# Kernel tuning notes

Hardware: AMD Instinct MI355X
Metric: run time of the kernel (lower is better)

The kernel has to match this reference:

```python
import jax, jax.numpy as jnp
import numpy as np
import math

B, S, E, H, F = 2, 2048, 1024, 16, 4096
D = E // H
EPS = 1e-5


def _layernorm(x, g, b):
    mu = jnp.mean(x, axis=-1, keepdims=True)
    var = jnp.mean(jnp.square(x - mu), axis=-1, keepdims=True)
    return (x - mu) * jax.lax.rsqrt(var + EPS) * g + b


def _xavier(k, fan_in, fan_out):
    limit = math.sqrt(6.0 / (fan_in + fan_out))
    return jax.random.uniform(k, (fan_in, fan_out), jnp.float32, -limit, limit)


def setup_inputs() -> dict:
    key = jax.random.key(0)
    ks = jax.random.split(key, 8)
    x = jax.random.normal(ks[0], (B, S, E), jnp.float32)
    # causal mask: 1 where attendable, 0 where masked (masked_fill at mask==0)
    mask = jnp.tril(jnp.ones((S, S), jnp.int32))[None, None]  # [1,1,S,S]
    return {
        "x": x,
        "mask": mask,
        "Wq": _xavier(ks[1], E, E), "bq": jnp.zeros((E,), jnp.float32),
        "Wk": _xavier(ks[2], E, E), "bk": jnp.zeros((E,), jnp.float32),
        "Wv": _xavier(ks[3], E, E), "bv": jnp.zeros((E,), jnp.float32),
        "Wo": _xavier(ks[4], E, E), "bo": jnp.zeros((E,), jnp.float32),
        "W1": _xavier(ks[5], E, F), "b1": jnp.zeros((F,), jnp.float32),
        "W2": _xavier(ks[6], F, E), "b2": jnp.zeros((E,), jnp.float32),
        "ln1_g": jnp.ones((E,), jnp.float32), "ln1_b": jnp.zeros((E,), jnp.float32),
        "ln2_g": jnp.ones((E,), jnp.float32), "ln2_b": jnp.zeros((E,), jnp.float32),
    }


def reference(x, mask, Wq, bq, Wk, bk, Wv, bv, Wo, bo, W1, b1, W2, b2,
              ln1_g, ln1_b, ln2_g, ln2_b):
    n = _layernorm(x, ln1_g, ln1_b)
    # project and split heads: [B,S,E] -> [B,H,S,D]
    def heads(w, b):
        return (n @ w + b).reshape(B, S, H, D).transpose(0, 2, 1, 3)
    Q, K, V = heads(Wq, bq), heads(Wk, bk), heads(Wv, bv)
    scores = jnp.einsum('bhsd,bhtd->bhst', Q, K) / math.sqrt(D)  # [B,H,S,S]
    scores = jnp.where(mask == 0, jnp.float32(-1e9), scores)
    attn = jax.nn.softmax(scores, axis=-1)
    ctx = jnp.einsum('bhst,bhtd->bhsd', attn, V)
    ctx = ctx.transpose(0, 2, 1, 3).reshape(B, S, E)
    attn_out = ctx @ Wo + bo
    x = _layernorm(x + attn_out, ln2_g, ln2_b)
    ffn = jax.nn.gelu(x @ W1 + b1, approximate=False) @ W2 + b2
    return x + ffn
```

## Files before the change

### kernel.cpp

```cpp
#include <hip/hip_runtime.h>
#include <cmath>

typedef unsigned short u16;
typedef unsigned int u32;
typedef __bf16 bf16x8 __attribute__((ext_vector_type(8)));
typedef float f32x4 __attribute__((ext_vector_type(4)));

#define SEQ 2048
#define EMB 1024
#define NHEAD 16
#define HDIM 64
#define FFDIM 4096
#define NBATCH 2
#define QKVLD 3072
#define PWS 68

#define QSCALE 0.18033688011112042f

__device__ __forceinline__ u16 f2bf(float f) {
  u32 u = __float_as_uint(f);
  u32 r = u + 0x7fffu + ((u >> 16) & 1u);
  return (u16)(r >> 16);
}

__device__ __forceinline__ float ex2(float x) {
#if __has_builtin(__builtin_amdgcn_exp2f)
  return __builtin_amdgcn_exp2f(x);
#else
  return exp2f(x);
#endif
}

__device__ __forceinline__ float geluf(float x) {
  float u = 0.7978845608028654f * (x + 0.044715f * x * x * x);
  float e = ex2(2.8853900817779268f * u);
  return x - x / (e + 1.0f);
}

__device__ __forceinline__ void gload16(const void* g, void* l) {
  __builtin_amdgcn_global_load_lds(
      (const __attribute__((address_space(1))) unsigned int*)g,
      (__attribute__((address_space(3))) unsigned int*)l, 16, 0, 0);
}

__device__ __forceinline__ u32 lds_addr(const void* p) {
  return (u32)(size_t)(const __attribute__((address_space(3))) void*)p;
}

template <int IMM>
__device__ __forceinline__ bf16x8 dsr16(u32 a) {
  bf16x8 r;
  asm volatile("ds_read_b128 %0, %1 offset:%2" : "=v"(r) : "v"(a), "n"(IMM));
  return r;
}

__global__ __launch_bounds__(256)
void wtrans_kernel(const float* __restrict__ W, u16* __restrict__ WT, int K, int N) {
  __shared__ float tile[32][33];
  int tx = threadIdx.x & 31, ty = threadIdx.x >> 5;
  int n0 = blockIdx.x * 32, k0 = blockIdx.y * 32;
#pragma unroll
  for (int i = 0; i < 32; i += 8)
    tile[ty + i][tx] = W[(size_t)(k0 + ty + i) * N + (n0 + tx)];
  __syncthreads();
#pragma unroll
  for (int i = 0; i < 32; i += 8)
    WT[(size_t)(n0 + ty + i) * K + (k0 + tx)] = f2bf(tile[tx][ty + i]);
}

__global__ __launch_bounds__(256)
void wtrans4_kernel(const float* __restrict__ W0, const float* __restrict__ W1_,
                    const float* __restrict__ W2_, const float* __restrict__ W3,
                    u16* __restrict__ Dqkv, u16* __restrict__ Do) {
  __shared__ float tile[32][33];
  int z = blockIdx.z;
  const float* W = (z == 0) ? W0 : (z == 1) ? W1_ : (z == 2) ? W2_ : W3;
  u16* D = (z < 3) ? (Dqkv + (size_t)z * EMB * EMB) : Do;
  int tx = threadIdx.x & 31, ty = threadIdx.x >> 5;
  int n0 = blockIdx.x * 32, k0 = blockIdx.y * 32;
#pragma unroll
  for (int i = 0; i < 32; i += 8)
    tile[ty + i][tx] = W[(size_t)(k0 + ty + i) * EMB + (n0 + tx)];
  __syncthreads();
#pragma unroll
  for (int i = 0; i < 32; i += 8)
    D[(size_t)(n0 + ty + i) * EMB + (k0 + tx)] = f2bf(tile[tx][ty + i]);
}

__global__ __launch_bounds__(256)
void vtrans_kernel(const u16* __restrict__ QKV, u16* __restrict__ Vt) {
  __shared__ u16 tile[64 * 72];
  int bh = blockIdx.y, b = bh >> 4, h = bh & 15;
  int s0 = blockIdx.x * 64;
  const u16* src = QKV + (size_t)b * SEQ * QKVLD + 2048 + (size_t)h * HDIM;
  int tid = threadIdx.x;
#pragma unroll
  for (int cc = 0; cc < 2; ++cc) {
    int c = tid + cc * 256;
    int s = c >> 3, d0 = (c & 7) * 8;
    uint4 v = *(const uint4*)(src + (size_t)(s0 + s) * QKVLD + d0);
    *(uint4*)(&tile[s * 72 + d0]) = v;
  }
  __syncthreads();
  u16* dst = Vt + (size_t)bh * HDIM * SEQ;
#pragma unroll
  for (int cc = 0; cc < 2; ++cc) {
    int c = tid + cc * 256;
    int d = c >> 3, t0l = (c & 7) * 8;
    union { uint4 u; u16 s[8]; } ou;
#pragma unroll
    for (int j = 0; j < 8; ++j) ou.s[j] = tile[(t0l + j) * 72 + d];
    *(uint4*)(dst + (size_t)d * SEQ + s0 + t0l) = ou.u;
  }
}

__global__ __launch_bounds__(256)
void ln_kernel(const float* __restrict__ in, const float* __restrict__ gamma,
               const float* __restrict__ beta, u16* __restrict__ outb) {
  int w = threadIdx.x >> 6, lane = threadIdx.x & 63;
  int row = blockIdx.x * 4 + w;
  size_t base = (size_t)row * EMB;
  float4 v[4];
  float s = 0.f, q = 0.f;
#pragma unroll
  for (int j = 0; j < 4; ++j) {
    v[j] = *(const float4*)(in + base + j * 256 + lane * 4);
    s += v[j].x + v[j].y + v[j].z + v[j].w;
    q += v[j].x * v[j].x + v[j].y * v[j].y + v[j].z * v[j].z + v[j].w * v[j].w;
  }
#pragma unroll
  for (int off = 1; off < 64; off <<= 1) {
    s += __shfl_xor(s, off);
    q += __shfl_xor(q, off);
  }
  float mean = s * (1.0f / EMB);
  float var = q * (1.0f / EMB) - mean * mean;
  float rstd = rsqrtf(var + 1e-5f);
#pragma unroll
  for (int j = 0; j < 4; ++j) {
    int c = j * 256 + lane * 4;
    float4 g4 = *(const float4*)(gamma + c);
    float4 b4 = *(const float4*)(beta + c);
    ushort4 ob;
    ob.x = f2bf((v[j].x - mean) * rstd * g4.x + b4.x);
    ob.y = f2bf((v[j].y - mean) * rstd * g4.y + b4.y);
    ob.z = f2bf((v[j].z - mean) * rstd * g4.z + b4.z);
    ob.w = f2bf((v[j].w - mean) * rstd * g4.w + b4.w);
    *(ushort4*)(outb + base + c) = ob;
  }
}

__global__ __launch_bounds__(256)
void ln2f_kernel(const float* __restrict__ p, size_t pstride,
                 const float* __restrict__ bias, const float* __restrict__ resid,
                 const float* __restrict__ gamma, const float* __restrict__ beta,
                 u16* __restrict__ outb, float* __restrict__ outf) {
  int w = threadIdx.x >> 6, lane = threadIdx.x & 63;
  int row = blockIdx.x * 4 + w;
  size_t base = (size_t)row * EMB;
  float4 v[4];
  float s = 0.f, q = 0.f;
#pragma unroll
  for (int j = 0; j < 4; ++j) {
    int c = j * 256 + lane * 4;
    float4 a = *(const float4*)(p + base + c);
    float4 b = *(const float4*)(p + pstride + base + c);
    float4 r = *(const float4*)(resid + base + c);
    float4 bb = *(const float4*)(bias + c);
    v[j].x = a.x + b.x + r.x + bb.x;
    v[j].y = a.y + b.y + r.y + bb.y;
    v[j].z = a.z + b.z + r.z + bb.z;
    v[j].w = a.w + b.w + r.w + bb.w;
    s += v[j].x + v[j].y + v[j].z + v[j].w;
    q += v[j].x * v[j].x + v[j].y * v[j].y + v[j].z * v[j].z + v[j].w * v[j].w;
  }
#pragma unroll
  for (int off = 1; off < 64; off <<= 1) {
    s += __shfl_xor(s, off);
    q += __shfl_xor(q, off);
  }
  float mean = s * (1.0f / EMB);
  float var = q * (1.0f / EMB) - mean * mean;
  float rstd = rsqrtf(var + 1e-5f);
#pragma unroll
  for (int j = 0; j < 4; ++j) {
    int c = j * 256 + lane * 4;
    float4 g4 = *(const float4*)(gamma + c);
    float4 b4 = *(const float4*)(beta + c);
    float y0 = (v[j].x - mean) * rstd * g4.x + b4.x;
    float y1 = (v[j].y - mean) * rstd * g4.y + b4.y;
    float y2 = (v[j].z - mean) * rstd * g4.z + b4.z;
    float y3 = (v[j].w - mean) * rstd * g4.w + b4.w;
    ushort4 ob;
    ob.x = f2bf(y0); ob.y = f2bf(y1); ob.z = f2bf(y2); ob.w = f2bf(y3);
    *(ushort4*)(outb + base + c) = ob;
    *(float4*)(outf + base + c) = make_float4(y0, y1, y2, y3);
  }
}

__global__ __launch_bounds__(256)
void reduce2_kernel(const float* __restrict__ p, size_t pstride,
                    const float* __restrict__ bias, const float* __restrict__ resid,
                    float* __restrict__ out, int ncols) {
  size_t i = ((size_t)blockIdx.x * 256 + threadIdx.x) * 4;
  float4 a = *(const float4*)(p + i);
  float4 b = *(const float4*)(p + pstride + i);
  float4 r = *(const float4*)(resid + i);
  int col = (int)(i & (size_t)(ncols - 1));
  float4 bb = *(const float4*)(bias + col);
  float4 o;
  o.x = a.x + b.x + r.x + bb.x;
  o.y = a.y + b.y + r.y + bb.y;
  o.z = a.z + b.z + r.z + bb.z;
  o.w = a.w + b.w + r.w + bb.w;
  *(float4*)(out + i) = o;
}

__global__ __launch_bounds__(256)
void gemm_bt(const u16* __restrict__ A, const u16* __restrict__ BT,
             const float* __restrict__ bias, const float* __restrict__ bias2,
             const float* __restrict__ bias3, void* __restrict__ out,
             const float* __restrict__ resid, int M, int N, int K,
             int mode, float scale, int ksplit,
             float* __restrict__ partial, size_t pstride) {
  __shared__ __align__(16) u16 As[128 * 64];
  __shared__ __align__(16) u16 Bs[128 * 64];
  int tid = threadIdx.x;
  int lane = tid & 63, w = tid >> 6;
  int wm = w >> 1, wn = w & 1;
  int g = lane >> 4, lr = lane & 15;
  int m0 = blockIdx.y * 128, n0 = blockIdx.x * 128;
  int z = blockIdx.z;
  int kbeg = z * ksplit, kend = kbeg + ksplit;

  f32x4 acc[4][4];
#pragma unroll
  for (int mt = 0; mt < 4; ++mt)
#pragma unroll
    for (int nt = 0; nt < 4; ++nt) {
      acc[mt][nt][0] = 0.f; acc[mt][nt][1] = 0.f;
      acc[mt][nt][2] = 0.f; acc[mt][nt][3] = 0.f;
    }

  size_t ao[4], bo_[4];
  int lo[4];
#pragma unroll
  for (int cc = 0; cc < 4; ++cc) {
    int c = tid + cc * 256;
    int row = c >> 3, slot = c & 7;
    int gc = slot ^ (row & 7);
    ao[cc] = (size_t)(m0 + row) * K + gc * 8;
    bo_[cc] = (size_t)(n0 + row) * K + gc * 8;
    lo[cc] = c * 8;
  }
  int swz[2];
#pragma unroll
  for (int kk = 0; kk < 2; ++kk) swz[kk] = ((kk * 4 + g) ^ (lr & 7)) * 8;

  for (int k0 = kbeg; k0 < kend; k0 += 64) {
    __syncthreads();
#pragma unroll
    for (int cc = 0; cc < 4; ++cc) gload16(A + ao[cc] + k0, As + lo[cc]);
#pragma unroll
    for (int cc = 0; cc < 4; ++cc) gload16(BT + bo_[cc] + k0, Bs + lo[cc]);
    __syncthreads();
#pragma unroll
    for (int kk = 0; kk < 2; ++kk) {
      bf16x8 af[4], bfr[4];
#pragma unroll
      for (int mt = 0; mt < 4; ++mt)
        af[mt] = *(const bf16x8*)(As + (wm * 64 + mt * 16 + lr) * 64 + swz[kk]);
#pragma unroll
      for (int nt = 0; nt < 4; ++nt)
        bfr[nt] = *(const bf16x8*)(Bs + (wn * 64 + nt * 16 + lr) * 64 + swz[kk]);
#pragma unroll
      for (int mt = 0; mt < 4; ++mt)
#pragma unroll
        for (int nt = 0; nt < 4; ++nt)
          acc[mt][nt] = __builtin_amdgcn_mfma_f32_16x16x32_bf16(af[mt], bfr[nt], acc[mt][nt], 0, 0, 0);
    }
  }

  float* pz = partial + (size_t)z * pstride;
#pragma unroll
  for (int mt = 0; mt < 4; ++mt) {
    int row = m0 + wm * 64 + mt * 16 + g * 4;
#pragma unroll
    for (int nt = 0; nt < 4; ++nt) {
      int col = n0 + wn * 64 + nt * 16 + lr;
      float bcol;
      if (mode == 3) {
        int which = col >> 10;
        const float* bp = (which == 0) ? bias : (which == 1) ? bias2 : bias3;
        bcol = bp[col & 1023];
      } else if (mode != 4) {
        bcol = bias[col];
      } else {
        bcol = 0.f;
      }
#pragma unroll
      for (int r = 0; r < 4; ++r) {
        float vacc = acc[mt][nt][r] + bcol;
        size_t idx = (size_t)(row + r) * N + col;
        if (mode == 0)      ((u16*)out)[idx] = f2bf(vacc * scale);
        else if (mode == 1) ((u16*)out)[idx] = f2bf(geluf(vacc));
        else if (mode == 2) ((float*)out)[idx] = vacc + resid[idx];
        else if (mode == 3) ((u16*)out)[idx] = f2bf(col < 1024 ? vacc * QSCALE : vacc);
        else                pz[idx] = vacc;
      }
    }
  }
}


#define BARM __builtin_amdgcn_s_barrier()
#define VMWS asm volatile("s_waitcnt vmcnt(%0)" ::"n"(4 + RA))
#define VMW0 asm volatile("s_waitcnt vmcnt(0)")
#define NOSTG ((void)0)
#define NOWT ((void)0)

#define STG_A(t, d, kh)                                                       \
  { _Pragma("unroll")                                                         \
    for (int j = 0; j < RA; ++j)                                              \
      gload16(A + (size_t)sgA[j] + kbeg + (t) * 64 + (kh) * 32,               \
              As + ((d) * 2 + (kh)) * ABUF + slA[j]); }

#define STG_B(t, d, kh)                                                       \
  { _Pragma("unroll")                                                         \
    for (int j = 0; j < 2; ++j)                                               \
      gload16(BT + (size_t)sgB[j] + kbeg + (t) * 64 + (kh) * 32,              \
              Bs + ((d) * 2 + (kh)) * 8192 + slB[j]); }

#define PHASE(d, kk, mh, STAGE, WAITC)                                        \
  {                                                                           \
    const u32 bA = bB + ((d) * 2 + (kk)) * 16384;                             \
    const u32 aA = aB + ((d) * 2 + (kk)) * (ABUF * 2);                        \
    if ((mh) == 0) {                                                          \
      bfr[0] = dsr16<0>(bA);                                                  \
      bfr[1] = dsr16<1024>(bA);                                               \
      bfr[2] = dsr16<2048>(bA);                                               \
      bfr[3] = dsr16<3072>(bA);                                               \
    }                                                                         \
    bf16x8 af[MT2];                                                           \
    af[0] = dsr16<(((mh) * MT2 + 0) * 1024)>(aA);                             \
    af[1] = dsr16<(((mh) * MT2 + 1) * 1024)>(aA);                             \
    if constexpr (MT2 > 2) {                                                  \
      af[2] = dsr16<(((mh) * MT2 + 2) * 1024)>(aA);                           \
      af[3] = dsr16<(((mh) * MT2 + 3) * 1024)>(aA);                           \
    }                                                                         \
    STAGE;                                                                    \
    BARM;                                                                     \
    asm volatile("s_waitcnt lgkmcnt(0)");                                     \
    __builtin_amdgcn_sched_barrier(0);                                        \
    __builtin_amdgcn_s_setprio(1);                                            \
    _Pragma("unroll")                                                         \
    for (int mi = 0; mi < MT2; ++mi)                                          \
      _Pragma("unroll")                                                       \
      for (int nt = 0; nt < 4; ++nt)                                          \
        acc[(mh) * MT2 + mi][nt] = __builtin_amdgcn_mfma_f32_16x16x32_bf16(   \
            af[mi], bfr[nt], acc[(mh) * MT2 + mi][nt], 0, 0, 0);              \
    __builtin_amdgcn_s_setprio(0);                                            \
    WAITC;                                                                    \
    BARM;                                                                     \
  }

#define SUB2(d, kk, mh)                                                       \
  {                                                                           \
    const u32 bA = bB + ((d) * 2 + (kk)) * 16384;                             \
    const u32 aA = aB + ((d) * 2 + (kk)) * (ABUF * 2);                        \
    if ((mh) == 0) {                                                          \
      bfr[0] = dsr16<0>(bA);                                                  \
      bfr[1] = dsr16<1024>(bA);                                               \
      bfr[2] = dsr16<2048>(bA);                                               \
      bfr[3] = dsr16<3072>(bA);                                               \
    }                                                                         \
    bf16x8 af[MT2];                                                           \
    af[0] = dsr16<(((mh) * MT2 + 0) * 1024)>(aA);                             \
    af[1] = dsr16<(((mh) * MT2 + 1) * 1024)>(aA);                             \
    if constexpr (MT2 > 2) {                                                  \
      af[2] = dsr16<(((mh) * MT2 + 2) * 1024)>(aA);                           \
      af[3] = dsr16<(((mh) * MT2 + 3) * 1024)>(aA);                           \
    }                                                                         \
    asm volatile("s_waitcnt lgkmcnt(0)");                                     \
    __builtin_amdgcn_sched_barrier(0);                                        \
    __builtin_amdgcn_s_setprio(1);                                            \
    _Pragma("unroll")                                                         \
    for (int mi = 0; mi < MT2; ++mi)                                          \
      _Pragma("unroll")                                                       \
      for (int nt = 0; nt < 4; ++nt)                                          \
        acc[(mh) * MT2 + mi][nt] = __builtin_amdgcn_mfma_f32_16x16x32_bf16(   \
            af[mi], bfr[nt], acc[(mh) * MT2 + mi][nt], 0, 0, 0);              \
    __builtin_amdgcn_s_setprio(0);                                            \
  }

#define TILE2(t, d)                                                           \
  {                                                                           \
    if ((t) + 1 < nk) {                                                       \
      STG_B((t) + 1, (d) ^ 1, 0); STG_A((t) + 1, (d) ^ 1, 0);                 \
      STG_B((t) + 1, (d) ^ 1, 1); STG_A((t) + 1, (d) ^ 1, 1);                 \
    }                                                                         \
    SUB2(d, 0, 0) SUB2(d, 0, 1) SUB2(d, 1, 0) SUB2(d, 1, 1)                   \
    if ((t) + 1 < nk) { VMW0; }                                               \
    BARM;                                                                     \
  }

#define GEMM_EPILOGUE                                                         \
  float* pz = partial + (size_t)z * pstride;                                  \
  _Pragma("unroll")                                                           \
  for (int mt = 0; mt < MT; ++mt) {                                           \
    int row = m0 + wm * (BM / 2) + mt * 16 + g * 4;                           \
    _Pragma("unroll")                                                         \
    for (int nt = 0; nt < 4; ++nt) {                                          \
      int col = n0 + wn * 64 + nt * 16 + lr;                                  \
      float bcol;                                                             \
      if (mode == 3) {                                                        \
        int which = col >> 10;                                                \
        const float* bp = (which == 0) ? bias : (which == 1) ? bias2 : bias3; \
        bcol = bp[col & 1023];                                                \
      } else if (mode != 4) {                                                 \
        bcol = bias[col];                                                     \
      } else {                                                                \
        bcol = 0.f;                                                           \
      }                                                                       \
      _Pragma("unroll")                                                       \
      for (int r = 0; r < 4; ++r) {                                           \
        float vacc = acc[mt][nt][r] + bcol;                                   \
        size_t idx = (size_t)(row + r) * N + col;                             \
        if (mode == 0)      ((u16*)out)[idx] = f2bf(vacc * scale);            \
        else if (mode == 1) ((u16*)out)[idx] = f2bf(geluf(vacc));             \
        else if (mode == 2) ((float*)out)[idx] = vacc + resid[idx];           \
        else if (mode == 3) ((u16*)out)[idx] = f2bf(col < 1024 ? vacc * QSCALE : vacc); \
        else                pz[idx] = vacc;                                   \
      }                                                                       \
    }                                                                         \
  }

#define GEMM_PRELUDE                                                          \
  constexpr int MT = BM / 32;                                                 \
  constexpr int MT2 = MT / 2;                                                 \
  constexpr int RA = BM / 128;                                                \
  constexpr int ABUF = BM * 32;                                               \
  __shared__ __align__(16) u16 As[4 * ABUF];                                  \
  __shared__ __align__(16) u16 Bs[4 * 8192];                                  \
  int tid = threadIdx.x;                                                      \
  int lane = tid & 63, w = tid >> 6;                                          \
  int wm = w >> 2, wn = w & 3;                                                \
  int g = lane >> 4, lr = lane & 15;                                          \
  int m0 = blockIdx.y * BM, n0 = blockIdx.x * 256;                            \
  int z = blockIdx.z;                                                         \
  size_t kbeg = (size_t)z * ksplit;                                           \
  int nk = ksplit >> 6;                                                       \
  int phys = ((lr & 1) * 4 + g) ^ ((lr >> 1) & 7);                            \
  int aoff = wm * (BM / 2) * 32 + (lr >> 1) * 64 + phys * 8;                  \
  int boff = wn * 2048 + (lr >> 1) * 64 + phys * 8;                           \
  const u32 aB = lds_addr(As) + 2 * aoff;                                     \
  const u32 bB = lds_addr(Bs) + 2 * boff;                                     \
  int sgA[RA], slA[RA];                                                       \
  _Pragma("unroll")                                                           \
  for (int j = 0; j < RA; ++j) {                                              \
    int c = tid + j * 512;                                                    \
    int sr = c >> 3, ph = c & 7, l = ph ^ (sr & 7);                           \
    sgA[j] = (m0 + 2 * sr + (l >> 2)) * K + (l & 3) * 8;                      \
    slA[j] = c * 8;                                                           \
  }                                                                           \
  int sgB[2], slB[2];                                                         \
  _Pragma("unroll")                                                           \
  for (int j = 0; j < 2; ++j) {                                               \
    int c = tid + j * 512;                                                    \
    int sr = c >> 3, ph = c & 7, l = ph ^ (sr & 7);                           \
    sgB[j] = (n0 + 2 * sr + (l >> 2)) * K + (l & 3) * 8;                      \
    slB[j] = c * 8;                                                           \
  }                                                                           \
  f32x4 acc[MT][4];                                                           \
  _Pragma("unroll")                                                           \
  for (int mt = 0; mt < MT; ++mt)                                             \
    _Pragma("unroll")                                                         \
    for (int nt = 0; nt < 4; ++nt) {                                          \
      acc[mt][nt][0] = 0.f; acc[mt][nt][1] = 0.f;                             \
      acc[mt][nt][2] = 0.f; acc[mt][nt][3] = 0.f;                             \
    }                                                                         \
  bf16x8 bfr[4];

template <int BM>
__global__ __launch_bounds__(512, 2)
void gemm8(const u16* __restrict__ A, const u16* __restrict__ BT,
           const float* __restrict__ bias, const float* __restrict__ bias2,
           const float* __restrict__ bias3, void* __restrict__ out,
           const float* __restrict__ resid, int M, int N, int K,
           int mode, float scale, int ksplit,
           float* __restrict__ partial, size_t pstride) {
  GEMM_PRELUDE
  int npair = nk >> 1;

  STG_B(0, 0, 0); STG_A(0, 0, 0); STG_B(0, 0, 1); STG_A(0, 0, 1);
  STG_B(1, 1, 0); STG_A(1, 1, 0); STG_B(1, 1, 1);
  VMWS; BARM;

  for (int it = 0; it < npair - 1; ++it) {
    int t1 = 2 * it + 1, t2 = 2 * it + 2, t3 = 2 * it + 3;
    PHASE(0, 0, 0, STG_A(t1, 1, 1), NOWT)
    PHASE(0, 0, 1, STG_B(t2, 0, 0), NOWT)
    PHASE(0, 1, 0, STG_A(t2, 0, 0), NOWT)
    PHASE(0, 1, 1, STG_B(t2, 0, 1), VMWS)
    PHASE(1, 0, 0, STG_A(t2, 0, 1), NOWT)
    PHASE(1, 0, 1, STG_B(t3, 1, 0), NOWT)
    PHASE(1, 1, 0, STG_A(t3, 1, 0), NOWT)
    PHASE(1, 1, 1, STG_B(t3, 1, 1), VMWS)
  }
  {
    int t1 = nk - 1;
    PHASE(0, 0, 0, STG_A(t1, 1, 1), NOWT)
    PHASE(0, 0, 1, NOSTG, NOWT)
    PHASE(0, 1, 0, NOSTG, NOWT)
    PHASE(0, 1, 1, NOSTG, VMW0)
    PHASE(1, 0, 0, NOSTG, NOWT)
    PHASE(1, 0, 1, NOSTG, NOWT)
    PHASE(1, 1, 0, NOSTG, NOWT)
    PHASE(1, 1, 1, NOSTG, NOWT)
  }
  GEMM_EPILOGUE
}

template <int BM>
__global__ __launch_bounds__(512, 2)
void gemm2p(const u16* __restrict__ A, const u16* __restrict__ BT,
            const float* __restrict__ bias, const float* __restrict__ bias2,
            const float* __restrict__ bias3, void* __restrict__ out,
            const float* __restrict__ resid, int M, int N, int K,
            int mode, float scale, int ksplit,
            float* __restrict__ partial, size_t pstride) {
  GEMM_PRELUDE
  STG_B(0, 0, 0); STG_A(0, 0, 0); STG_B(0, 0, 1); STG_A(0, 0, 1);
  VMW0; BARM;

  int npair = nk >> 1;
  for (int tp = 0; tp < npair; ++tp) {
    int t0 = 2 * tp, t1 = t0 + 1;
    TILE2(t0, 0)
    TILE2(t1, 1)
  }
  GEMM_EPILOGUE
}

__shared__ __align__(16) u16 attn_Kt[64 * 64];
__shared__ __align__(16) u16 attn_VT[64 * 64];
__shared__ __align__(16) u16 attn_Pw[2][4][16 * PWS];

template <int S0>
__device__ __forceinline__ void attn_tile(
    int t0, const int* q0, int w, int g, int lr, const bf16x8& ones,
    bf16x8 (&qf)[2][2], f32x4 (&lacc)[2], f32x4 (&oacc)[2][4]) {
  f32x4 sacc[2][4];
#pragma unroll
  for (int s = S0; s < 2; ++s)
#pragma unroll
    for (int nt = 0; nt < 4; ++nt) {
      sacc[s][nt][0] = 0.f; sacc[s][nt][1] = 0.f;
      sacc[s][nt][2] = 0.f; sacc[s][nt][3] = 0.f;
    }
#pragma unroll
  for (int kk = 0; kk < 2; ++kk)
#pragma unroll
    for (int nt = 0; nt < 4; ++nt) {
      int sw = ((kk * 4 + g) ^ lr) & 7;
      bf16x8 bfr = *(const bf16x8*)(&attn_Kt[(nt * 16 + lr) * 64 + sw * 8]);
      if (S0 == 0)
        sacc[0][nt] = __builtin_amdgcn_mfma_f32_16x16x32_bf16(qf[0][kk], bfr, sacc[0][nt], 0, 0, 0);
      sacc[1][nt] = __builtin_amdgcn_mfma_f32_16x16x32_bf16(qf[1][kk], bfr, sacc[1][nt], 0, 0, 0);
    }

#pragma unroll
  for (int s = S0; s < 2; ++s) {
    bool diag = (t0 == q0[s]);
#pragma unroll
    for (int r = 0; r < 4; ++r) {
#pragma unroll
      for (int nt = 0; nt < 4; ++nt) {
        float pv = ex2(sacc[s][nt][r]);
        if (diag && (nt * 16 + lr > w * 16 + g * 4 + r)) pv = 0.f;
        attn_Pw[s][w][(g * 4 + r) * PWS + nt * 16 + lr] = f2bf(pv);
      }
    }
  }

#pragma unroll
  for (int kk = 0; kk < 2; ++kk) {
    bf16x8 pf0, pf1;
    if (S0 == 0) pf0 = *(const bf16x8*)(&attn_Pw[0][w][lr * PWS + kk * 32 + g * 8]);
    pf1 = *(const bf16x8*)(&attn_Pw[1][w][lr * PWS + kk * 32 + g * 8]);
#pragma unroll
    for (int nt = 0; nt < 4; ++nt) {
      int sw = ((kk * 4 + g) ^ lr) & 7;
      bf16x8 vf = *(const bf16x8*)(&attn_VT[(nt * 16 + lr) * 64 + sw * 8]);
      if (S0 == 0)
        oacc[0][nt] = __builtin_amdgcn_mfma_f32_16x16x32_bf16(pf0, vf, oacc[0][nt], 0, 0, 0);
      oacc[1][nt] = __builtin_amdgcn_mfma_f32_16x16x32_bf16(pf1, vf, oacc[1][nt], 0, 0, 0);
    }
    if (S0 == 0)
      lacc[0] = __builtin_amdgcn_mfma_f32_16x16x32_bf16(pf0, ones, lacc[0], 0, 0, 0);
    lacc[1] = __builtin_amdgcn_mfma_f32_16x16x32_bf16(pf1, ones, lacc[1], 0, 0, 0);
  }
}

__global__ __launch_bounds__(256)
void attn2_kernel(const u16* __restrict__ QKV, const u16* __restrict__ Vt,
                  u16* __restrict__ ctx) {
  int tid = threadIdx.x, lane = tid & 63, w = tid >> 6;
  int g = lane >> 4, lr = lane & 15;
  int bh = blockIdx.y, b = bh >> 4, h = bh & 15;
  int q0[2];
  q0[0] = blockIdx.x * 64;
  q0[1] = (SEQ / 64 - 1 - blockIdx.x) * 64;
  const u16* Qh = QKV + (size_t)b * SEQ * QKVLD + (size_t)h * HDIM;
  const u16* Kh = Qh + 1024;
  const u16* Vth = Vt + (size_t)bh * HDIM * SEQ;

  bf16x8 ones;
#pragma unroll
  for (int j = 0; j < 8; ++j) ones[j] = (__bf16)1.0f;

  bf16x8 qf[2][2];
#pragma unroll
  for (int s = 0; s < 2; ++s)
#pragma unroll
    for (int kk = 0; kk < 2; ++kk)
      qf[s][kk] = *(const bf16x8*)(Qh + (size_t)(q0[s] + w * 16 + lr) * QKVLD + kk * 32 + g * 8);

  f32x4 lacc[2];
  f32x4 oacc[2][4];
#pragma unroll
  for (int s = 0; s < 2; ++s) {
    lacc[s][0] = 0.f; lacc[s][1] = 0.f; lacc[s][2] = 0.f; lacc[s][3] = 0.f;
#pragma unroll
    for (int nt = 0; nt < 4; ++nt) {
      oacc[s][nt][0] = 0.f; oacc[s][nt][1] = 0.f;
      oacc[s][nt][2] = 0.f; oacc[s][nt][3] = 0.f;
    }
  }

  int c1 = tid, c2 = tid + 256;
  int t1 = c1 >> 3, ch1 = (c1 ^ t1) & 7;
  int t2 = c2 >> 3, ch2 = (c2 ^ t2) & 7;
  for (int t0 = 0; t0 <= q0[1]; t0 += 64) {
    __syncthreads();
    gload16(Kh + (size_t)(t0 + t1) * QKVLD + ch1 * 8, attn_Kt + c1 * 8);
    gload16(Kh + (size_t)(t0 + t2) * QKVLD + ch2 * 8, attn_Kt + c2 * 8);
    gload16(Vth + (size_t)t1 * SEQ + t0 + ch1 * 8, attn_VT + c1 * 8);
    gload16(Vth + (size_t)t2 * SEQ + t0 + ch2 * 8, attn_VT + c2 * 8);
    __syncthreads();

    if (t0 <= q0[0])
      attn_tile<0>(t0, q0, w, g, lr, ones, qf, lacc, oacc);
    else
      attn_tile<1>(t0, q0, w, g, lr, ones, qf, lacc, oacc);
  }

#pragma unroll
  for (int s = 0; s < 2; ++s) {
    int srow = q0[s] + w * 16 + g * 4;
    float inv[4];
#pragma unroll
    for (int r = 0; r < 4; ++r) inv[r] = 1.0f / lacc[s][r];
#pragma unroll
    for (int nt = 0; nt < 4; ++nt) {
      int col = h * HDIM + nt * 16 + lr;
#pragma unroll
      for (int r = 0; r < 4; ++r) {
        float o = oacc[s][nt][r] * inv[r];
        ctx[((size_t)b * SEQ + srow + r) * EMB + col] = f2bf(o);
      }
    }
  }
}

extern "C" void kernel_launch(void* const* d_in, const int* in_sizes, int n_in,
                              void* d_out, int out_size, void* d_ws, size_t ws_size,
                              hipStream_t stream) {
  const float* x    = (const float*)d_in[0];
  const float* Wq   = (const float*)d_in[2];
  const float* bq   = (const float*)d_in[3];
  const float* Wk   = (const float*)d_in[4];
  const float* bk   = (const float*)d_in[5];
  const float* Wv   = (const float*)d_in[6];
  const float* bv   = (const float*)d_in[7];
  const float* Wo   = (const float*)d_in[8];
  const float* bo   = (const float*)d_in[9];
  const float* W1   = (const float*)d_in[10];
  const float* b1   = (const float*)d_in[11];
  const float* W2   = (const float*)d_in[12];
  const float* b2   = (const float*)d_in[13];
  const float* ln1g = (const float*)d_in[14];
  const float* ln1b = (const float*)d_in[15];
  const float* ln2g = (const float*)d_in[16];
  const float* ln2b = (const float*)d_in[17];

  char* ws = (char*)d_ws;
  u16* WqkvT = (u16*)(ws + ((size_t)0 << 20));
  u16* WoT   = (u16*)(ws + ((size_t)6 << 20));
  u16* W1T   = (u16*)(ws + ((size_t)8 << 20));
  u16* W2T   = (u16*)(ws + ((size_t)16 << 20));
  u16* xb    = (u16*)(ws + ((size_t)24 << 20));
  u16* QKVb  = (u16*)(ws + ((size_t)32 << 20));
  u16* ctxb  = (u16*)(ws + ((size_t)56 << 20));
  float* x2f = (float*)(ws + ((size_t)48 << 20));
  u16* x2b   = xb;
  u16* VtG   = (u16*)(ws + ((size_t)64 << 20));
  float* pWo = (float*)(ws + ((size_t)64 << 20));
  u16* h1    = (u16*)(ws + ((size_t)64 << 20));
  float* pF2 = (float*)(ws + ((size_t)0 << 20));

  dim3 blk(256);
  dim3 blk512(512);
  const int M = NBATCH * SEQ;

  wtrans4_kernel<<<dim3(32, 32, 4), blk, 0, stream>>>(Wq, Wk, Wv, Wo, WqkvT, WoT);
  wtrans_kernel<<<dim3(128, 32), blk, 0, stream>>>(W1, W1T, EMB, FFDIM);
  wtrans_kernel<<<dim3(32, 128), blk, 0, stream>>>(W2, W2T, FFDIM, EMB);

  ln_kernel<<<M / 4, blk, 0, stream>>>(x, ln1g, ln1b, xb);

  gemm_bt<<<dim3(QKVLD / 128, M / 128), blk, 0, stream>>>(
      xb, WqkvT, bq, bk, bv, QKVb, nullptr, M, QKVLD, EMB, 3, 1.0f, EMB, nullptr, 0);

  vtrans_kernel<<<dim3(SEQ / 64, NBATCH * NHEAD), blk, 0, stream>>>(QKVb, VtG);

  attn2_kernel<<<dim3(SEQ / 128, NBATCH * NHEAD), blk, 0, stream>>>(QKVb, VtG, ctxb);

  gemm8<128><<<dim3(EMB / 256, M / 128, 2), blk512, 0, stream>>>(
      ctxb, WoT, nullptr, nullptr, nullptr, nullptr, nullptr, M, EMB, EMB, 4, 1.0f,
      EMB / 2, pWo, (size_t)4 << 20);

  ln2f_kernel<<<M / 4, blk, 0, stream>>>(pWo, (size_t)4 << 20, bo, x, ln2g, ln2b,
                                         x2b, x2f);

  gemm2p<256><<<dim3(FFDIM / 256, M / 256), blk512, 0, stream>>>(
      x2b, W1T, b1, nullptr, nullptr, h1, nullptr, M, FFDIM, EMB, 1, 1.0f, EMB,
      nullptr, 0);

  gemm8<128><<<dim3(EMB / 256, M / 128, 2), blk512, 0, stream>>>(
      h1, W2T, nullptr, nullptr, nullptr, nullptr, nullptr, M, EMB, FFDIM, 4, 1.0f,
      FFDIM / 2, pF2, (size_t)8 << 20);
  reduce2_kernel<<<M * EMB / 1024, blk, 0, stream>>>(pF2, (size_t)8 << 20, b2, x2f,
                                                     (float*)d_out, EMB);
}
```

Baseline: 407.4 us.

## Add XCD-aware block swizzle to GEMMs and use gemm8 for FFN1

Adds an XCD swizzle that remaps the linear workgroup index so that consecutive tiles land on the same XCD. This is meant to improve L2 reuse of A and B tiles across the chiplets. The FFN1 GEMM now uses the 8-phase pipelined gemm8 kernel in place of the removed gemm2p double-tile variant. The swizzle assumes the workgroup count divides evenly by 8, and it also changes tile order in the QKV and split-K GEMMs.

Measured after the change: 400.5 us. About the same (-1.7%).

```diff
diff --git a/kernel.cpp b/kernel.cpp
--- a/kernel.cpp
+++ b/kernel.cpp
@@ -52,6 +52,15 @@
   bf16x8 r;
   asm volatile("ds_read_b128 %0, %1 offset:%2" : "=v"(r) : "v"(a), "n"(IMM));
   return r;
+}
+
+__device__ __forceinline__ void xcd_swizzle(int gx, int gy, int& bx, int& by) {
+  int nwg = gx * gy;
+  int lin = blockIdx.x + gx * blockIdx.y;
+  int q = nwg >> 3;
+  int nl = (lin & 7) * q + (lin >> 3);
+  bx = nl % gx;
+  by = nl / gx;
 }
 
 __global__ __launch_bounds__(256)
@@ -229,7 +238,9 @@
   int lane = tid & 63, w = tid >> 6;
   int wm = w >> 1, wn = w & 1;
   int g = lane >> 4, lr = lane & 15;
-  int m0 = blockIdx.y * 128, n0 = blockIdx.x * 128;
+  int bx, by;
+  xcd_swizzle(gridDim.x, gridDim.y, bx, by);
+  int m0 = by * 128, n0 = bx * 128;
   int z = blockIdx.z;
   int kbeg = z * ksplit, kend = kbeg + ksplit;
 
@@ -364,46 +375,6 @@
     BARM;                                                                     \
   }
 
-#define SUB2(d, kk, mh)                                                       \
-  {                                                                           \
-    const u32 bA = bB + ((d) * 2 + (kk)) * 16384;                             \
-    const u32 aA = aB + ((d) * 2 + (kk)) * (ABUF * 2);                        \
-    if ((mh) == 0) {                                                          \
-      bfr[0] = dsr16<0>(bA);                                                  \
-      bfr[1] = dsr16<1024>(bA);                                               \
-      bfr[2] = dsr16<2048>(bA);                                               \
-      bfr[3] = dsr16<3072>(bA);                                               \
-    }                                                                         \
-    bf16x8 af[MT2];                                                           \
-    af[0] = dsr16<(((mh) * MT2 + 0) * 1024)>(aA);                             \
-    af[1] = dsr16<(((mh) * MT2 + 1) * 1024)>(aA);                             \
-    if constexpr (MT2 > 2) {                                                  \
-      af[2] = dsr16<(((mh) * MT2 + 2) * 1024)>(aA);                           \
-      af[3] = dsr16<(((mh) * MT2 + 3) * 1024)>(aA);                           \
-    }                                                                         \
-    asm volatile("s_waitcnt lgkmcnt(0)");                                     \
-    __builtin_amdgcn_sched_barrier(0);                                        \
-    __builtin_amdgcn_s_setprio(1);                                            \
-    _Pragma("unroll")                                                         \
-    for (int mi = 0; mi < MT2; ++mi)                                          \
-      _Pragma("unroll")                                                       \
-      for (int nt = 0; nt < 4; ++nt)                                          \
-        acc[(mh) * MT2 + mi][nt] = __builtin_amdgcn_mfma_f32_16x16x32_bf16(   \
-            af[mi], bfr[nt], acc[(mh) * MT2 + mi][nt], 0, 0, 0);              \
-    __builtin_amdgcn_s_setprio(0);                                            \
-  }
-
-#define TILE2(t, d)                                                           \
-  {                                                                           \
-    if ((t) + 1 < nk) {                                                       \
-      STG_B((t) + 1, (d) ^ 1, 0); STG_A((t) + 1, (d) ^ 1, 0);                 \
-      STG_B((t) + 1, (d) ^ 1, 1); STG_A((t) + 1, (d) ^ 1, 1);                 \
-    }                                                                         \
-    SUB2(d, 0, 0) SUB2(d, 0, 1) SUB2(d, 1, 0) SUB2(d, 1, 1)                   \
-    if ((t) + 1 < nk) { VMW0; }                                               \
-    BARM;                                                                     \
-  }
-
 #define GEMM_EPILOGUE                                                         \
   float* pz = partial + (size_t)z * pstride;                                  \
   _Pragma("unroll")                                                           \
@@ -446,7 +417,9 @@
   int lane = tid & 63, w = tid >> 6;                                          \
   int wm = w >> 2, wn = w & 3;                                                \
   int g = lane >> 4, lr = lane & 15;                                          \
-  int m0 = blockIdx.y * BM, n0 = blockIdx.x * 256;                            \
+  int bx, by;                                                                 \
+  xcd_swizzle(gridDim.x, gridDim.y, bx, by);                                  \
+  int m0 = by * BM, n0 = bx * 256;                                            \
   int z = blockIdx.z;                                                         \
   size_t kbeg = (size_t)z * ksplit;                                           \
   int nk = ksplit >> 6;                                                       \
@@ -521,27 +494,6 @@
   GEMM_EPILOGUE
 }
 
-template <int BM>
-__global__ __launch_bounds__(512, 2)
-void gemm2p(const u16* __restrict__ A, const u16* __restrict__ BT,
-            const float* __restrict__ bias, const float* __restrict__ bias2,
-            const float* __restrict__ bias3, void* __restrict__ out,
-            const float* __restrict__ resid, int M, int N, int K,
-            int mode, float scale, int ksplit,
-            float* __restrict__ partial, size_t pstride) {
-  GEMM_PRELUDE
-  STG_B(0, 0, 0); STG_A(0, 0, 0); STG_B(0, 0, 1); STG_A(0, 0, 1);
-  VMW0; BARM;
-
-  int npair = nk >> 1;
-  for (int tp = 0; tp < npair; ++tp) {
-    int t0 = 2 * tp, t1 = t0 + 1;
-    TILE2(t0, 0)
-    TILE2(t1, 1)
-  }
-  GEMM_EPILOGUE
-}
-
 __shared__ __align__(16) u16 attn_Kt[64 * 64];
 __shared__ __align__(16) u16 attn_VT[64 * 64];
 __shared__ __align__(16) u16 attn_Pw[2][4][16 * PWS];
@@ -733,7 +685,7 @@
   ln2f_kernel<<<M / 4, blk, 0, stream>>>(pWo, (size_t)4 << 20, bo, x, ln2g, ln2b,
                                          x2b, x2f);
 
-  gemm2p<256><<<dim3(FFDIM / 256, M / 256), blk512, 0, stream>>>(
+  gemm8<256><<<dim3(FFDIM / 256, M / 256), blk512, 0, stream>>>(
       x2b, W1T, b1, nullptr, nullptr, h1, nullptr, M, FFDIM, EMB, 1, 1.0f, EMB,
       nullptr, 0);
 
```
